# Optimization experiments

Hardware: AMD Instinct MI355X
Metric: run time of the kernel (lower is better)

Reference implementation:

```python
import jax, jax.numpy as jnp
import numpy as np

BSZ, SEQ, DIM = 4, 4096, 1024
MEASURE_DIM = 64
TOPK = 16
NUM_TARGETS = 1


def fwht(x):
    """Fast Walsh-Hadamard transform over last dim (power of two), orthonormal scaling."""
    n = x.shape[-1]
    y = x
    h = 1
    while h < n:
        y = y.reshape(*y.shape[:-1], -1, 2, h)
        a, b = y[..., 0, :], y[..., 1, :]
        y = jnp.concatenate((a + b, a - b), axis=-1)
        y = y.reshape(*x.shape[:-1], n)
        h *= 2
    return y * (n ** -0.5)


def setup_inputs() -> dict:
    key = jax.random.key(0)
    kx, kg, ka, kt, ks, kp = jax.random.split(key, 6)
    x = jax.random.normal(kx, (BSZ, SEQ, DIM), dtype=jnp.float32)
    gates = jax.random.uniform(kg, (BSZ, NUM_TARGETS, MEASURE_DIM), dtype=jnp.float32) + 0.5
    alpha = jax.random.uniform(ka, (BSZ, NUM_TARGETS, 1), dtype=jnp.float32) * 0.1
    tau = jax.random.uniform(kt, (BSZ, NUM_TARGETS, 1), dtype=jnp.float32) * 0.02
    signs = jnp.where(jax.random.uniform(ks, (DIM,)) > 0.5, 1.0, -1.0).astype(jnp.float32)
    perm = jax.random.permutation(kp, DIM).astype(jnp.int32)
    inv_perm = jnp.argsort(perm).astype(jnp.int32)
    return {"x": x, "gates": gates, "alpha": alpha, "tau": tau,
            "signs": signs, "perm": perm, "inv_perm": inv_perm, "target_idx": 0}


def reference(x, gates, alpha, tau, signs, perm, inv_perm, target_idx):
    signs_ = signs.astype(x.dtype)
    # ---- sense: sign flip -> permute -> FWHT -> truncate ----
    y = jnp.take((x * signs_[None, None, :]), perm, axis=-1)
    z = fwht(y)[..., :MEASURE_DIM]  # [B, S, m]
    # ---- shrink (topk mode) ----
    gate = gates[:, target_idx][:, None, :]            # [B, 1, m]
    alpha_t = alpha[:, target_idx][:, None, :]         # [B, 1, 1]
    tau_t = jnp.abs(tau[:, target_idx])[:, None, :]    # [B, 1, 1]
    gated = gate * z
    agated = jnp.abs(gated)
    _, idx = jax.lax.top_k(agated, TOPK)               # [B, S, k]
    mask = jax.nn.one_hot(idx, MEASURE_DIM, dtype=gated.dtype).sum(-2)  # [B, S, m]
    sparse = jnp.where((mask > 0) & (agated >= tau_t), gated, jnp.zeros_like(gated))
    zs = alpha_t * sparse
    # ---- reconstruct: pad -> FWHT -> inverse permute -> sign flip ----
    full = jnp.zeros((*zs.shape[:-1], DIM), dtype=zs.dtype).at[..., :MEASURE_DIM].set(zs)
    r = jnp.take(fwht(full), inv_perm, axis=-1) * signs_[None, None, :]
    return x + r
```

## Files before the change

### kernel.cpp

```cpp
#include <hip/hip_runtime.h>

#define SEQ 4096
#define DIM 1024
#define MD 64
#define TOPK 16
#define WPB 2
#define RPW 2
#define RPB (WPB * RPW)

typedef float nfloat4 __attribute__((ext_vector_type(4)));

__global__ __launch_bounds__(WPB * 64) void csa_kernel(
    const float* __restrict__ x,
    const float* __restrict__ gates,
    const float* __restrict__ alpha,
    const float* __restrict__ tau,
    const float* __restrict__ signs,
    const int*   __restrict__ perm,
    const int*   __restrict__ inv_perm,
    const int*   __restrict__ target_idx,
    float*       __restrict__ out)
{
    __shared__ float y[RPB][DIM];

    const int lane = threadIdx.x & 63;
    const int wv   = threadIdx.x >> 6;
    const int r0   = (blockIdx.x * WPB + wv) * RPW;
    const int b    = r0 >> 12;

    float4 xv0[4], xv1[4];
    #pragma unroll
    for (int c = 0; c < 4; ++c) {
        const float4 sg = ((const float4*)signs)[c * 64 + lane];
        xv0[c] = ((const float4*)(x + (size_t)(r0 + 0) * DIM))[c * 64 + lane];
        xv1[c] = ((const float4*)(x + (size_t)(r0 + 1) * DIM))[c * 64 + lane];
        float4 y0, y1;
        y0.x = xv0[c].x * sg.x; y0.y = xv0[c].y * sg.y;
        y0.z = xv0[c].z * sg.z; y0.w = xv0[c].w * sg.w;
        y1.x = xv1[c].x * sg.x; y1.y = xv1[c].y * sg.y;
        y1.z = xv1[c].z * sg.z; y1.w = xv1[c].w * sg.w;
        ((float4*)y[wv * RPW + 0])[c * 64 + lane] = y0;
        ((float4*)y[wv * RPW + 1])[c * 64 + lane] = y1;
    }

    float s0 = 0.f, s1 = 0.f;
    #pragma unroll
    for (int k = 0; k < 16; ++k) {
        const int p = perm[lane + 64 * k];
        s0 += y[wv * RPW + 0][p];
        s1 += y[wv * RPW + 1][p];
    }

    float v0 = s0, v1 = s1;
    #pragma unroll
    for (int bit = 1; bit < MD; bit <<= 1) {
        const float o0 = __shfl_xor(v0, bit, 64);
        const float o1 = __shfl_xor(v1, bit, 64);
        v0 = (lane & bit) ? (o0 - v0) : (v0 + o0);
        v1 = (lane & bit) ? (o1 - v1) : (v1 + o1);
    }

    const int   ti   = target_idx[0];
    const float gate = gates[(b + ti) * MD + lane];
    const float tauv = fabsf(tau[b + ti]);
    const float al   = alpha[b + ti];

    const float g0 = gate * v0 * 0.03125f;
    const float g1 = gate * v1 * 0.03125f;
    const float ag0 = fabsf(g0), ag1 = fabsf(g1);

    const unsigned ka0 = __float_as_uint(ag0);
    const unsigned ka1 = __float_as_uint(ag1);
    unsigned T0 = 0u, T1 = 0u;
    #pragma unroll
    for (int bit = 30; bit >= 0; --bit) {
        const unsigned c0 = T0 | (1u << bit);
        const unsigned c1 = T1 | (1u << bit);
        if (__popcll(__ballot(ka0 >= c0)) >= TOPK) T0 = c0;
        if (__popcll(__ballot(ka1 >= c1)) >= TOPK) T1 = c1;
    }
    const int ngt0 = __popcll(__ballot(ka0 > T0));
    const int ngt1 = __popcll(__ballot(ka1 > T1));
    const unsigned long long lm = (1ull << lane) - 1ull;
    const int er0 = __popcll(__ballot(ka0 == T0) & lm);
    const int er1 = __popcll(__ballot(ka1 == T1) & lm);
    const bool k0 = (ka0 > T0) || ((ka0 == T0) && (er0 < TOPK - ngt0));
    const bool k1 = (ka1 > T1) || ((ka1 == T1) && (er1 < TOPK - ngt1));

    float zs0 = (k0 && ag0 >= tauv) ? al * g0 : 0.f;
    float zs1 = (k1 && ag1 >= tauv) ? al * g1 : 0.f;

    #pragma unroll
    for (int bit = 1; bit < MD; bit <<= 1) {
        const float o0 = __shfl_xor(zs0, bit, 64);
        const float o1 = __shfl_xor(zs1, bit, 64);
        zs0 = (lane & bit) ? (o0 - zs0) : (zs0 + o0);
        zs1 = (lane & bit) ? (o1 - zs1) : (zs1 + o1);
    }
    const int wb0 = __float_as_int(zs0 * 0.03125f);
    const int wb1 = __float_as_int(zs1 * 0.03125f);

    nfloat4* out0 = (nfloat4*)(out + (size_t)(r0 + 0) * DIM);
    nfloat4* out1 = (nfloat4*)(out + (size_t)(r0 + 1) * DIM);
    #pragma unroll
    for (int c = 0; c < 4; ++c) {
        const float4 sg = ((const float4*)signs)[c * 64 + lane];
        const int4   ip = ((const int4*)inv_perm)[c * 64 + lane];
        const int a0 = (ip.x & 63) << 2, a1 = (ip.y & 63) << 2;
        const int a2 = (ip.z & 63) << 2, a3 = (ip.w & 63) << 2;

        nfloat4 o0, o1;
        o0.x = xv0[c].x + sg.x * __int_as_float(__builtin_amdgcn_ds_bpermute(a0, wb0));
        o0.y = xv0[c].y + sg.y * __int_as_float(__builtin_amdgcn_ds_bpermute(a1, wb0));
        o0.z = xv0[c].z + sg.z * __int_as_float(__builtin_amdgcn_ds_bpermute(a2, wb0));
        o0.w = xv0[c].w + sg.w * __int_as_float(__builtin_amdgcn_ds_bpermute(a3, wb0));
        o1.x = xv1[c].x + sg.x * __int_as_float(__builtin_amdgcn_ds_bpermute(a0, wb1));
        o1.y = xv1[c].y + sg.y * __int_as_float(__builtin_amdgcn_ds_bpermute(a1, wb1));
        o1.z = xv1[c].z + sg.z * __int_as_float(__builtin_amdgcn_ds_bpermute(a2, wb1));
        o1.w = xv1[c].w + sg.w * __int_as_float(__builtin_amdgcn_ds_bpermute(a3, wb1));

        __builtin_nontemporal_store(o0, &out0[c * 64 + lane]);
        __builtin_nontemporal_store(o1, &out1[c * 64 + lane]);
    }
}

extern "C" void kernel_launch(void* const* d_in, const int* in_sizes, int n_in,
                              void* d_out, int out_size, void* d_ws, size_t ws_size,
                              hipStream_t stream) {
    const float* x        = (const float*)d_in[0];
    const float* gates    = (const float*)d_in[1];
    const float* alpha    = (const float*)d_in[2];
    const float* tau      = (const float*)d_in[3];
    const float* signs    = (const float*)d_in[4];
    const int*   perm     = (const int*)d_in[5];
    const int*   inv_perm = (const int*)d_in[6];
    const int*   tgt      = (const int*)d_in[7];
    float*       out      = (float*)d_out;

    const int rows = 4 * SEQ;
    csa_kernel<<<rows / RPB, WPB * 64, 0, stream>>>(x, gates, alpha, tau, signs,
                                                    perm, inv_perm, tgt, out);
}
```

Before: 124.2 us.

## Reconstruct output via scatter-add into LDS instead of holding x in registers

Stops keeping the two loaded x rows in registers across the whole kernel. The sign-flipped rows stay in shared memory, the reconstruction term is added back by scattering through perm into that shared buffer, and the output is read back from LDS and sign-multiplied, with no bpermute and no inv_perm loads. This lowers register pressure and removes the inv_perm global reads. In exchange it adds 32 scattered LDS writes plus LDS reads per lane, and relies on signs being ±1 so that sign*(sign*x + w) equals x + sign*w.

```diff
diff --git a/kernel.cpp b/kernel.cpp
--- a/kernel.cpp
+++ b/kernel.cpp
@@ -28,27 +28,31 @@
     const int r0   = (blockIdx.x * WPB + wv) * RPW;
     const int b    = r0 >> 12;
 
-    float4 xv0[4], xv1[4];
+    float* y0 = y[wv * RPW + 0];
+    float* y1 = y[wv * RPW + 1];
+
     #pragma unroll
     for (int c = 0; c < 4; ++c) {
         const float4 sg = ((const float4*)signs)[c * 64 + lane];
-        xv0[c] = ((const float4*)(x + (size_t)(r0 + 0) * DIM))[c * 64 + lane];
-        xv1[c] = ((const float4*)(x + (size_t)(r0 + 1) * DIM))[c * 64 + lane];
-        float4 y0, y1;
-        y0.x = xv0[c].x * sg.x; y0.y = xv0[c].y * sg.y;
-        y0.z = xv0[c].z * sg.z; y0.w = xv0[c].w * sg.w;
-        y1.x = xv1[c].x * sg.x; y1.y = xv1[c].y * sg.y;
-        y1.z = xv1[c].z * sg.z; y1.w = xv1[c].w * sg.w;
-        ((float4*)y[wv * RPW + 0])[c * 64 + lane] = y0;
-        ((float4*)y[wv * RPW + 1])[c * 64 + lane] = y1;
+        const float4 xa = ((const float4*)(x + (size_t)(r0 + 0) * DIM))[c * 64 + lane];
+        const float4 xb = ((const float4*)(x + (size_t)(r0 + 1) * DIM))[c * 64 + lane];
+        float4 a, bq;
+        a.x  = xa.x * sg.x; a.y  = xa.y * sg.y; a.z  = xa.z * sg.z; a.w  = xa.w * sg.w;
+        bq.x = xb.x * sg.x; bq.y = xb.y * sg.y; bq.z = xb.z * sg.z; bq.w = xb.w * sg.w;
+        ((float4*)y0)[c * 64 + lane] = a;
+        ((float4*)y1)[c * 64 + lane] = bq;
     }
 
+    int   pk[16];
+    float ya[16], yb[16];
     float s0 = 0.f, s1 = 0.f;
     #pragma unroll
     for (int k = 0; k < 16; ++k) {
-        const int p = perm[lane + 64 * k];
-        s0 += y[wv * RPW + 0][p];
-        s1 += y[wv * RPW + 1][p];
+        pk[k] = perm[lane + 64 * k];
+        ya[k] = y0[pk[k]];
+        yb[k] = y1[pk[k]];
+        s0 += ya[k];
+        s1 += yb[k];
     }
 
     float v0 = s0, v1 = s1;
@@ -97,28 +101,25 @@
         zs0 = (lane & bit) ? (o0 - zs0) : (zs0 + o0);
         zs1 = (lane & bit) ? (o1 - zs1) : (zs1 + o1);
     }
-    const int wb0 = __float_as_int(zs0 * 0.03125f);
-    const int wb1 = __float_as_int(zs1 * 0.03125f);
+    const float w0 = zs0 * 0.03125f;
+    const float w1 = zs1 * 0.03125f;
+
+    #pragma unroll
+    for (int k = 0; k < 16; ++k) {
+        y0[pk[k]] = ya[k] + w0;
+        y1[pk[k]] = yb[k] + w1;
+    }
 
     nfloat4* out0 = (nfloat4*)(out + (size_t)(r0 + 0) * DIM);
     nfloat4* out1 = (nfloat4*)(out + (size_t)(r0 + 1) * DIM);
     #pragma unroll
     for (int c = 0; c < 4; ++c) {
         const float4 sg = ((const float4*)signs)[c * 64 + lane];
-        const int4   ip = ((const int4*)inv_perm)[c * 64 + lane];
-        const int a0 = (ip.x & 63) << 2, a1 = (ip.y & 63) << 2;
-        const int a2 = (ip.z & 63) << 2, a3 = (ip.w & 63) << 2;
-
+        const float4 t0 = ((const float4*)y0)[c * 64 + lane];
+        const float4 t1 = ((const float4*)y1)[c * 64 + lane];
         nfloat4 o0, o1;
-        o0.x = xv0[c].x + sg.x * __int_as_float(__builtin_amdgcn_ds_bpermute(a0, wb0));
-        o0.y = xv0[c].y + sg.y * __int_as_float(__builtin_amdgcn_ds_bpermute(a1, wb0));
-        o0.z = xv0[c].z + sg.z * __int_as_float(__builtin_amdgcn_ds_bpermute(a2, wb0));
-        o0.w = xv0[c].w + sg.w * __int_as_float(__builtin_amdgcn_ds_bpermute(a3, wb0));
-        o1.x = xv1[c].x + sg.x * __int_as_float(__builtin_amdgcn_ds_bpermute(a0, wb1));
-        o1.y = xv1[c].y + sg.y * __int_as_float(__builtin_amdgcn_ds_bpermute(a1, wb1));
-        o1.z = xv1[c].z + sg.z * __int_as_float(__builtin_amdgcn_ds_bpermute(a2, wb1));
-        o1.w = xv1[c].w + sg.w * __int_as_float(__builtin_amdgcn_ds_bpermute(a3, wb1));
-
+        o0.x = sg.x * t0.x; o0.y = sg.y * t0.y; o0.z = sg.z * t0.z; o0.w = sg.w * t0.w;
+        o1.x = sg.x * t1.x; o1.y = sg.y * t1.y; o1.z = sg.z * t1.z; o1.w = sg.w * t1.w;
         __builtin_nontemporal_store(o0, &out0[c * 64 + lane]);
         __builtin_nontemporal_store(o1, &out1[c * 64 + lane]);
     }
```

Measured after the change: 123.6 us. Within noise of the previous version (-0.5%).
